# Performance work log

Hardware: AMD Instinct MI355X
Metric: run time of the kernel (lower is better)

## Reference

```python
import jax, jax.numpy as jnp
import numpy as np

COMMITMENT_COST = 0.25


def setup_inputs() -> dict:
    key = jax.random.key(0)
    k1, k2 = jax.random.split(key)
    inputs = jax.random.normal(k1, (64, 1024, 128), dtype=jnp.float32)
    # torch.rand init -> uniform [0, 1)
    codewords = jax.random.uniform(k2, (1024, 128), dtype=jnp.float32)
    return {"inputs": inputs, "codewords": codewords}


def reference(inputs, codewords):
    sg = jax.lax.stop_gradient
    D = codewords.shape[-1]
    flat = inputs.reshape(-1, D)  # (N, D)
    distances = (
        jnp.sum(flat * flat, axis=1, keepdims=True)
        - 2.0 * flat @ codewords.T
        + jnp.sum(codewords * codewords, axis=1)
    )  # (N, K)
    encoding_indices = jnp.argmin(distances, axis=1)  # (N,)
    quantized = codewords[encoding_indices].reshape(inputs.shape)

    quantizing_loss = jnp.mean((sg(quantized) - inputs) ** 2)
    commitment_loss = jnp.mean((quantized - sg(inputs)) ** 2)
    loss = quantizing_loss + COMMITMENT_COST * commitment_loss

    # straight-through estimator
    quantized = inputs + sg(quantized - inputs)
    return quantized, encoding_indices[:, None], loss
```

## Files before the change

kernel.cpp:

```cpp
#include <hip/hip_runtime.h>
#include <stdint.h>


typedef short     bf16x8 __attribute__((ext_vector_type(8)));
typedef float     f32x4  __attribute__((ext_vector_type(4)));
typedef unsigned short u16x8 __attribute__((ext_vector_type(8)));
typedef unsigned short u16x2 __attribute__((ext_vector_type(2)));

constexpr int N_ROWS = 65536;
constexpr int K_CODES = 1024;
constexpr int D = 128;
constexpr float MARGIN = 0.03f;

__device__ __forceinline__ unsigned short f32_to_bf16_rn(float f) {
    unsigned u = __float_as_uint(f);
    unsigned r = (u + 0x7FFFu + ((u >> 16) & 1u)) >> 16;
    return (unsigned short)r;
}
__device__ __forceinline__ float bf16_to_f32(unsigned short h) {
    return __uint_as_float(((unsigned)h) << 16);
}

__device__ __forceinline__ void gload_lds16(const void* g, void* l) {
    __builtin_amdgcn_global_load_lds(
        (const __attribute__((address_space(1))) unsigned int*)g,
        (__attribute__((address_space(3))) unsigned int*)l, 16, 0, 0);
}

__global__ __launch_bounds__(64) void vq_prep_cw(const float* __restrict__ cw,
                                                 unsigned short* __restrict__ Cp,
                                                 float* __restrict__ cnorm,
                                                 int* __restrict__ rcnt) {
    const int k = blockIdx.x;
    const int lane = threadIdx.x;
    float2 v = reinterpret_cast<const float2*>(cw + (size_t)k * D)[lane];
    float s = v.x * v.x + v.y * v.y;
#pragma unroll
    for (int off = 32; off; off >>= 1) s += __shfl_down(s, off, 64);
    if (lane == 0) cnorm[k] = s;
    if (lane == 0 && k == 0) *rcnt = 0;

    unsigned short hx = f32_to_bf16_rn(v.x), hy = f32_to_bf16_rn(v.y);
    unsigned short lx = f32_to_bf16_rn(v.x - bf16_to_f32(hx));
    unsigned short ly = f32_to_bf16_rn(v.y - bf16_to_f32(hy));
    size_t off0 = (size_t)k * D + lane * 2;
    u16x2 hv; hv[0] = hx; hv[1] = hy;
    u16x2 lv; lv[0] = lx; lv[1] = ly;
    *reinterpret_cast<u16x2*>(Cp + off0) = hv;
    *reinterpret_cast<u16x2*>(Cp + 131072 + off0) = lv;
}

__global__ __launch_bounds__(256, 3) void vq_argmin_mfma(
    const float* __restrict__ x,
    const unsigned short* __restrict__ Cp,
    const float* __restrict__ cnorm,
    float* __restrict__ half_bv,
    float* __restrict__ half_bv2,
    int* __restrict__ half_bi,
    float* __restrict__ xnorm) {
    __shared__ unsigned char Bs[2][2][8192];

    const int tid = threadIdx.x;
    const int wave = tid >> 6;
    const int lane = tid & 63;
    const int l15 = lane & 15;
    const int lg = lane >> 4;
    const int tile = blockIdx.x >> 1;
    const int khalf = blockIdx.x & 1;
    const int wrow = tile * 128 + wave * 32;

    const char* Cpb = reinterpret_cast<const char*>(Cp);
    auto stageB = [&](int c, int b) {
#pragma unroll
        for (int u = 0; u < 4; ++u) {
            int t = wave * 4 + u;
            int pl = t >> 3;
            int cwl = (t & 7) * 4 + lg;
            int q = l15 * 16;
            const char* src = Cpb + pl * 262144 + khalf * 131072
                              + ((size_t)(c * 32 + cwl)) * 256 + (q ^ ((cwl & 7) << 4));
            void* dst = (void*)&Bs[b][pl][(t & 7) * 1024];
            gload_lds16(src, dst);
        }
    };
    stageB(0, 0);

    bf16x8 A[2][4][2];
    float xn[2] = {0.f, 0.f};
#pragma unroll
    for (int r2 = 0; r2 < 2; ++r2) {
        const float* xr0 = x + (size_t)(wrow + r2 * 16 + l15) * D;
#pragma unroll
        for (int s = 0; s < 4; ++s) {
            const float4* xf = reinterpret_cast<const float4*>(xr0 + s * 32 + lg * 8);
            float4 f0 = xf[0];
            float4 f1 = xf[1];
            float in[8] = {f0.x, f0.y, f0.z, f0.w, f1.x, f1.y, f1.z, f1.w};
            u16x8 hv, lv;
#pragma unroll
            for (int e = 0; e < 8; ++e) {
                xn[r2] += in[e] * in[e];
                unsigned short h = f32_to_bf16_rn(in[e]);
                hv[e] = h;
                lv[e] = f32_to_bf16_rn(in[e] - bf16_to_f32(h));
            }
            A[r2][s][0] = *reinterpret_cast<bf16x8*>(&hv);
            A[r2][s][1] = *reinterpret_cast<bf16x8*>(&lv);
        }
    }
#pragma unroll
    for (int r2 = 0; r2 < 2; ++r2) {
        xn[r2] += __shfl_xor(xn[r2], 16, 64);
        xn[r2] += __shfl_xor(xn[r2], 32, 64);
        if (khalf == 0 && lg == 0) xnorm[wrow + r2 * 16 + l15] = xn[r2];
    }

    float bv[2][4], bv2[2][4];
    int bi_[2][4];
#pragma unroll
    for (int r2 = 0; r2 < 2; ++r2)
#pragma unroll
        for (int i = 0; i < 4; ++i) { bv[r2][i] = 3.4e38f; bv2[r2][i] = 3.4e38f; bi_[r2][i] = 0; }

    const int cb = l15 * 256;
    const int swz = (l15 & 7) << 4;
    int kb[4];
#pragma unroll
    for (int s = 0; s < 4; ++s) kb[s] = (s * 64 + lg * 16) ^ swz;

    asm volatile("s_waitcnt vmcnt(0)" ::: "memory");
    __syncthreads();

    for (int c = 0; c < 16; ++c) {
        const int buf = c & 1;
        if (c < 15) stageB(c + 1, buf ^ 1);

        f32x4 acc[2][2];
#pragma unroll
        for (int r2 = 0; r2 < 2; ++r2)
#pragma unroll
            for (int j = 0; j < 2; ++j) acc[r2][j] = (f32x4)(0.f);

#pragma unroll
        for (int s = 0; s < 4; ++s) {
            bf16x8 bh[2], bl[2];
#pragma unroll
            for (int j = 0; j < 2; ++j) {
                int ad = j * 4096 + cb + kb[s];
                bh[j] = *reinterpret_cast<const bf16x8*>(&Bs[buf][0][ad]);
                bl[j] = *reinterpret_cast<const bf16x8*>(&Bs[buf][1][ad]);
            }
#pragma unroll
            for (int r2 = 0; r2 < 2; ++r2)
#pragma unroll
                for (int j = 0; j < 2; ++j) {
                    acc[r2][j] = __builtin_amdgcn_mfma_f32_16x16x32_bf16(
                        A[r2][s][0], bh[j], acc[r2][j], 0, 0, 0);
                    acc[r2][j] = __builtin_amdgcn_mfma_f32_16x16x32_bf16(
                        A[r2][s][0], bl[j], acc[r2][j], 0, 0, 0);
                    acc[r2][j] = __builtin_amdgcn_mfma_f32_16x16x32_bf16(
                        A[r2][s][1], bh[j], acc[r2][j], 0, 0, 0);
                }
        }

#pragma unroll
        for (int j = 0; j < 2; ++j) {
            int col = khalf * 512 + c * 32 + j * 16 + l15;
            float cn = cnorm[col];
#pragma unroll
            for (int r2 = 0; r2 < 2; ++r2)
#pragma unroll
                for (int i = 0; i < 4; ++i) {
                    float sc = cn - 2.f * acc[r2][j][i];
                    if (sc < bv[r2][i]) {
                        bv2[r2][i] = bv[r2][i];
                        bv[r2][i] = sc;
                        bi_[r2][i] = col;
                    } else if (sc < bv2[r2][i]) {
                        bv2[r2][i] = sc;
                    }
                }
        }
        asm volatile("s_waitcnt vmcnt(0)" ::: "memory");
        __syncthreads();
    }

#pragma unroll
    for (int r2 = 0; r2 < 2; ++r2)
#pragma unroll
        for (int i = 0; i < 4; ++i) {
            float v = bv[r2][i], v2 = bv2[r2][i];
            int ix = bi_[r2][i];
#pragma unroll
            for (int off = 1; off < 16; off <<= 1) {
                float ov = __shfl_xor(v, off, 64);
                float ov2 = __shfl_xor(v2, off, 64);
                int oi = __shfl_xor(ix, off, 64);
                float nv2 = fminf(fminf(v2, ov2), fmaxf(v, ov));
                if (ov < v || (ov == v && oi < ix)) { v = ov; ix = oi; }
                v2 = nv2;
            }
            if (l15 == 0) {
                int row = wrow + r2 * 16 + lg * 4 + i;
                int o = khalf * N_ROWS + row;
                half_bv[o] = v;
                half_bv2[o] = v2;
                half_bi[o] = ix;
            }
        }
}

__global__ __launch_bounds__(256) void vq_merge(const float* __restrict__ cw,
                                                const float* __restrict__ half_bv,
                                                const float* __restrict__ half_bv2,
                                                const int* __restrict__ half_bi,
                                                const float* __restrict__ xnorm,
                                                float* __restrict__ out_idx_f,
                                                float* __restrict__ qout,
                                                float* __restrict__ rowloss,
                                                int* __restrict__ rcnt,
                                                int* __restrict__ rrows) {
    const int t = threadIdx.x;
    const int row = blockIdx.x * 8 + (t >> 5);
    const int d4 = t & 31;

    float v0 = half_bv[row], v0b = half_bv2[row];
    int i0 = half_bi[row];
    float v1 = half_bv[N_ROWS + row], v1b = half_bv2[N_ROWS + row];
    int i1 = half_bi[N_ROWS + row];

    bool take0 = (v0 < v1) || (v0 == v1 && i0 <= i1);
    float best = take0 ? v0 : v1;
    int bidx = take0 ? i0 : i1;
    float second = take0 ? fminf(v1, v0b) : fminf(v0, v1b);

    float4 q4 = reinterpret_cast<const float4*>(cw)[(size_t)bidx * 32 + d4];
    reinterpret_cast<float4*>(qout)[(size_t)row * 32 + d4] = q4;

    if (d4 == 0) {
        out_idx_f[row] = (float)bidx;
        rowloss[row] = xnorm[row] + best;
        if (second - best < MARGIN) {
            int p = atomicAdd(rcnt, 1);
            rrows[p] = row;
        }
    }
}

__global__ __launch_bounds__(256) void vq_repair(const float* __restrict__ x,
                                                 const float* __restrict__ cw,
                                                 const float* __restrict__ cnorm,
                                                 const float* __restrict__ xnorm,
                                                 const int* __restrict__ rcnt,
                                                 const int* __restrict__ rrows,
                                                 float* __restrict__ out_idx_f,
                                                 float* __restrict__ qout,
                                                 float* __restrict__ rowloss) {
    __shared__ float xs[16][132];
    __shared__ int rowids[16];
    __shared__ float sval[16][16];
    __shared__ int sidx[16][16];
    __shared__ int fidx[16];

    const int t = threadIdx.x;
    const int count = *rcnt;
    const float4* cw4 = reinterpret_cast<const float4*>(cw);

    for (int g = blockIdx.x; g * 16 < count; g += 256) {
        int nrows = min(16, count - g * 16);
        __syncthreads();
        if (t < 16) rowids[t] = rrows[g * 16 + (t < nrows ? t : 0)];
        __syncthreads();
        for (int i = t; i < 512; i += 256) {
            int r = i >> 5, d4 = i & 31;
            *reinterpret_cast<float4*>(&xs[r][d4 * 4]) =
                reinterpret_cast<const float4*>(x)[(size_t)rowids[r] * 32 + d4];
        }
        __syncthreads();

        const int r = t & 15;
        const int qq = t >> 4;
        float bv = 3.4e38f;
        int bi = 0;
#pragma unroll 2
        for (int kt = 0; kt < 8; ++kt) {
            float a[8] = {0.f, 0.f, 0.f, 0.f, 0.f, 0.f, 0.f, 0.f};
            int k0 = qq * 64 + kt * 8;
            for (int d4 = 0; d4 < 32; ++d4) {
                float4 xv = *reinterpret_cast<const float4*>(&xs[r][d4 * 4]);
#pragma unroll
                for (int kk = 0; kk < 8; ++kk) {
                    float4 cv = cw4[(size_t)(k0 + kk) * 32 + d4];
                    a[kk] += xv.x * cv.x + xv.y * cv.y + xv.z * cv.z + xv.w * cv.w;
                }
            }
#pragma unroll
            for (int kk = 0; kk < 8; ++kk) {
                int k = k0 + kk;
                float sc = cnorm[k] - 2.f * a[kk];
                if (sc < bv) { bv = sc; bi = k; }
            }
        }
        sval[r][qq] = bv;
        sidx[r][qq] = bi;
        __syncthreads();
        if (t < 16) {
            float fv = sval[t][0];
            int fi = sidx[t][0];
#pragma unroll
            for (int q2 = 1; q2 < 16; ++q2) {
                float v = sval[t][q2];
                int ii = sidx[t][q2];
                if (v < fv || (v == fv && ii < fi)) { fv = v; fi = ii; }
            }
            fidx[t] = fi;
            if (t < nrows) {
                int row = rowids[t];
                out_idx_f[row] = (float)fi;
                rowloss[row] = xnorm[row] + fv;
            }
        }
        __syncthreads();
        for (int i = t; i < 512; i += 256) {
            int rr = i >> 5, d4 = i & 31;
            float4 q4 = cw4[(size_t)fidx[rr] * 32 + d4];
            reinterpret_cast<float4*>(qout)[(size_t)rowids[rr] * 32 + d4] = q4;
        }
    }
}

__global__ __launch_bounds__(1024) void vq_loss_final(const float* __restrict__ rowloss,
                                                      float* __restrict__ out_loss) {
    double s = 0.0;
    for (int i = threadIdx.x; i < N_ROWS; i += 1024) s += (double)rowloss[i];
#pragma unroll
    for (int off = 32; off; off >>= 1) s += __shfl_down(s, off, 64);
    __shared__ double wsum[16];
    if ((threadIdx.x & 63) == 0) wsum[threadIdx.x >> 6] = s;
    __syncthreads();
    if (threadIdx.x == 0) {
        double tot = 0.0;
#pragma unroll
        for (int i = 0; i < 16; ++i) tot += wsum[i];
        *out_loss = (float)(tot * (1.25 / (double)((size_t)N_ROWS * D)));
    }
}

extern "C" void kernel_launch(void* const* d_in, const int* in_sizes, int n_in,
                              void* d_out, int out_size, void* d_ws, size_t ws_size,
                              hipStream_t stream) {
    const float* x = (const float*)d_in[0];
    const float* cw = (const float*)d_in[1];

    float* qout = (float*)d_out;
    float* out_idx_f = qout + (size_t)N_ROWS * D;
    float* out_loss = out_idx_f + N_ROWS;

    char* w = (char*)d_ws;
    unsigned short* Cp = (unsigned short*)w;          w += 524288;
    float* cnorm = (float*)w;                         w += 4096;
    int* rcnt = (int*)w;                              w += 256;
    int* rrows = (int*)w;                             w += 262144;
    float* half_bv = (float*)w;                       w += 524288;
    float* half_bv2 = (float*)w;                      w += 524288;
    int* half_bi = (int*)w;                           w += 524288;
    float* xnorm = (float*)w;                         w += 262144;
    float* rowloss = (float*)w;                       w += 262144;

    vq_prep_cw<<<K_CODES, 64, 0, stream>>>(cw, Cp, cnorm, rcnt);
    vq_argmin_mfma<<<(N_ROWS / 128) * 2, 256, 0, stream>>>(
        x, Cp, cnorm, half_bv, half_bv2, half_bi, xnorm);
    vq_merge<<<N_ROWS / 8, 256, 0, stream>>>(
        cw, half_bv, half_bv2, half_bi, xnorm, out_idx_f, qout, rowloss, rcnt, rrows);
    vq_repair<<<256, 256, 0, stream>>>(
        x, cw, cnorm, xnorm, rcnt, rrows, out_idx_f, qout, rowloss);
    vq_loss_final<<<1, 1024, 0, stream>>>(rowloss, out_loss);
}
```

Before: 256.5 us.

## Triple-buffer codebook staging, fuse loss reduction into merge/repair, shrink repair margin

The argmin kernel moves from double to triple buffering of codebook chunks. It waits with a partial vmcnt and raises wave priority around the MFMA block, so loads run further ahead of compute. The merge kernel handles 256 rows per block and accumulates the loss sum with a double atomic. Repair blocks add their delta to the same accumulator, and the final loss kernel becomes a single scalar write. The repair margin drops from 0.03 to 0.01, so fewer rows are rechecked in fp32, with some risk of index mismatches for near-ties given the bf16x3 precision.

```diff
diff --git a/kernel.cpp b/kernel.cpp
--- a/kernel.cpp
+++ b/kernel.cpp
@@ -10,7 +10,7 @@
 constexpr int N_ROWS = 65536;
 constexpr int K_CODES = 1024;
 constexpr int D = 128;
-constexpr float MARGIN = 0.03f;
+constexpr float MARGIN = 0.01f;
 
 __device__ __forceinline__ unsigned short f32_to_bf16_rn(float f) {
     unsigned u = __float_as_uint(f);
@@ -30,7 +30,8 @@
 __global__ __launch_bounds__(64) void vq_prep_cw(const float* __restrict__ cw,
                                                  unsigned short* __restrict__ Cp,
                                                  float* __restrict__ cnorm,
-                                                 int* __restrict__ rcnt) {
+                                                 int* __restrict__ rcnt,
+                                                 double* __restrict__ acc) {
     const int k = blockIdx.x;
     const int lane = threadIdx.x;
     float2 v = reinterpret_cast<const float2*>(cw + (size_t)k * D)[lane];
@@ -38,7 +39,7 @@
 #pragma unroll
     for (int off = 32; off; off >>= 1) s += __shfl_down(s, off, 64);
     if (lane == 0) cnorm[k] = s;
-    if (lane == 0 && k == 0) *rcnt = 0;
+    if (lane == 0 && k == 0) { *rcnt = 0; *acc = 0.0; }
 
     unsigned short hx = f32_to_bf16_rn(v.x), hy = f32_to_bf16_rn(v.y);
     unsigned short lx = f32_to_bf16_rn(v.x - bf16_to_f32(hx));
@@ -58,7 +59,7 @@
     float* __restrict__ half_bv2,
     int* __restrict__ half_bi,
     float* __restrict__ xnorm) {
-    __shared__ unsigned char Bs[2][2][8192];
+    __shared__ unsigned char Bs[3][2][8192];
 
     const int tid = threadIdx.x;
     const int wave = tid >> 6;
@@ -115,6 +116,8 @@
         if (khalf == 0 && lg == 0) xnorm[wrow + r2 * 16 + l15] = xn[r2];
     }
 
+    stageB(1, 1);
+
     float bv[2][4], bv2[2][4];
     int bi_[2][4];
 #pragma unroll
@@ -128,19 +131,14 @@
 #pragma unroll
     for (int s = 0; s < 4; ++s) kb[s] = (s * 64 + lg * 16) ^ swz;
 
-    asm volatile("s_waitcnt vmcnt(0)" ::: "memory");
-    __syncthreads();
-
-    for (int c = 0; c < 16; ++c) {
-        const int buf = c & 1;
-        if (c < 15) stageB(c + 1, buf ^ 1);
-
+    auto computeChunk = [&](int c, int buf) {
         f32x4 acc[2][2];
 #pragma unroll
         for (int r2 = 0; r2 < 2; ++r2)
 #pragma unroll
             for (int j = 0; j < 2; ++j) acc[r2][j] = (f32x4)(0.f);
 
+        __builtin_amdgcn_s_setprio(1);
 #pragma unroll
         for (int s = 0; s < 4; ++s) {
             bf16x8 bh[2], bl[2];
@@ -162,6 +160,7 @@
                         A[r2][s][1], bh[j], acc[r2][j], 0, 0, 0);
                 }
         }
+        __builtin_amdgcn_s_setprio(0);
 
 #pragma unroll
         for (int j = 0; j < 2; ++j) {
@@ -181,9 +180,21 @@
                     }
                 }
         }
-        asm volatile("s_waitcnt vmcnt(0)" ::: "memory");
-        __syncthreads();
-    }
+    };
+
+    int cur = 0;
+    for (int c = 0; c < 15; ++c) {
+        asm volatile("s_waitcnt vmcnt(4)\n\ts_barrier" ::: "memory");
+        if (c < 14) {
+            int stg = cur + 2;
+            if (stg >= 3) stg -= 3;
+            stageB(c + 2, stg);
+        }
+        computeChunk(c, cur);
+        cur = (cur == 2) ? 0 : cur + 1;
+    }
+    asm volatile("s_waitcnt vmcnt(0)\n\ts_barrier" ::: "memory");
+    computeChunk(15, cur);
 
 #pragma unroll
     for (int r2 = 0; r2 < 2; ++r2)
@@ -219,32 +230,44 @@
                                                 float* __restrict__ qout,
                                                 float* __restrict__ rowloss,
                                                 int* __restrict__ rcnt,
-                                                int* __restrict__ rrows) {
+                                                int* __restrict__ rrows,
+                                                double* __restrict__ acc) {
     const int t = threadIdx.x;
-    const int row = blockIdx.x * 8 + (t >> 5);
     const int d4 = t & 31;
-
-    float v0 = half_bv[row], v0b = half_bv2[row];
-    int i0 = half_bi[row];
-    float v1 = half_bv[N_ROWS + row], v1b = half_bv2[N_ROWS + row];
-    int i1 = half_bi[N_ROWS + row];
-
-    bool take0 = (v0 < v1) || (v0 == v1 && i0 <= i1);
-    float best = take0 ? v0 : v1;
-    int bidx = take0 ? i0 : i1;
-    float second = take0 ? fminf(v1, v0b) : fminf(v0, v1b);
-
-    float4 q4 = reinterpret_cast<const float4*>(cw)[(size_t)bidx * 32 + d4];
-    reinterpret_cast<float4*>(qout)[(size_t)row * 32 + d4] = q4;
-
-    if (d4 == 0) {
-        out_idx_f[row] = (float)bidx;
-        rowloss[row] = xnorm[row] + best;
-        if (second - best < MARGIN) {
-            int p = atomicAdd(rcnt, 1);
-            rrows[p] = row;
-        }
-    }
+    double lsum = 0.0;
+
+    for (int it = 0; it < 32; ++it) {
+        int row = blockIdx.x * 256 + it * 8 + (t >> 5);
+        float v0 = half_bv[row], v0b = half_bv2[row];
+        int i0 = half_bi[row];
+        float v1 = half_bv[N_ROWS + row], v1b = half_bv2[N_ROWS + row];
+        int i1 = half_bi[N_ROWS + row];
+
+        bool take0 = (v0 < v1) || (v0 == v1 && i0 <= i1);
+        float best = take0 ? v0 : v1;
+        int bidx = take0 ? i0 : i1;
+        float second = take0 ? fminf(v1, v0b) : fminf(v0, v1b);
+
+        float4 q4 = reinterpret_cast<const float4*>(cw)[(size_t)bidx * 32 + d4];
+        reinterpret_cast<float4*>(qout)[(size_t)row * 32 + d4] = q4;
+
+        if (d4 == 0) {
+            out_idx_f[row] = (float)bidx;
+            float rl = xnorm[row] + best;
+            rowloss[row] = rl;
+            lsum += (double)rl;
+            if (second - best < MARGIN) {
+                int p = atomicAdd(rcnt, 1);
+                rrows[p] = row;
+            }
+        }
+    }
+#pragma unroll
+    for (int off = 32; off; off >>= 1) lsum += __shfl_down(lsum, off, 64);
+    __shared__ double wsum[4];
+    if ((t & 63) == 0) wsum[t >> 6] = lsum;
+    __syncthreads();
+    if (t == 0) atomicAdd(acc, wsum[0] + wsum[1] + wsum[2] + wsum[3]);
 }
 
 __global__ __launch_bounds__(256) void vq_repair(const float* __restrict__ x,
@@ -255,7 +278,8 @@
                                                  const int* __restrict__ rrows,
                                                  float* __restrict__ out_idx_f,
                                                  float* __restrict__ qout,
-                                                 float* __restrict__ rowloss) {
+                                                 float* __restrict__ rowloss,
+                                                 double* __restrict__ acc) {
     __shared__ float xs[16][132];
     __shared__ int rowids[16];
     __shared__ float sval[16][16];
@@ -265,8 +289,9 @@
     const int t = threadIdx.x;
     const int count = *rcnt;
     const float4* cw4 = reinterpret_cast<const float4*>(cw);
-
-    for (int g = blockIdx.x; g * 16 < count; g += 256) {
+    double dsum = 0.0;
+
+    for (int g = blockIdx.x; g * 16 < count; g += 512) {
         int nrows = min(16, count - g * 16);
         __syncthreads();
         if (t < 16) rowids[t] = rrows[g * 16 + (t < nrows ? t : 0)];
@@ -317,7 +342,10 @@
             if (t < nrows) {
                 int row = rowids[t];
                 out_idx_f[row] = (float)fi;
-                rowloss[row] = xnorm[row] + fv;
+                float nrl = xnorm[row] + fv;
+                float orl = rowloss[row];
+                rowloss[row] = nrl;
+                dsum += (double)nrl - (double)orl;
             }
         }
         __syncthreads();
@@ -327,23 +355,20 @@
             reinterpret_cast<float4*>(qout)[(size_t)rowids[rr] * 32 + d4] = q4;
         }
     }
-}
-
-__global__ __launch_bounds__(1024) void vq_loss_final(const float* __restrict__ rowloss,
-                                                      float* __restrict__ out_loss) {
-    double s = 0.0;
-    for (int i = threadIdx.x; i < N_ROWS; i += 1024) s += (double)rowloss[i];
-#pragma unroll
-    for (int off = 32; off; off >>= 1) s += __shfl_down(s, off, 64);
-    __shared__ double wsum[16];
-    if ((threadIdx.x & 63) == 0) wsum[threadIdx.x >> 6] = s;
+#pragma unroll
+    for (int off = 32; off; off >>= 1) dsum += __shfl_down(dsum, off, 64);
+    __shared__ double wsum[4];
+    if ((t & 63) == 0) wsum[t >> 6] = dsum;
     __syncthreads();
-    if (threadIdx.x == 0) {
-        double tot = 0.0;
-#pragma unroll
-        for (int i = 0; i < 16; ++i) tot += wsum[i];
-        *out_loss = (float)(tot * (1.25 / (double)((size_t)N_ROWS * D)));
-    }
+    if (t == 0) {
+        double b = wsum[0] + wsum[1] + wsum[2] + wsum[3];
+        if (b != 0.0) atomicAdd(acc, b);
+    }
+}
+
+__global__ void vq_loss_final(const double* __restrict__ acc,
+                              float* __restrict__ out_loss) {
+    *out_loss = (float)(*acc * (1.25 / (double)((size_t)N_ROWS * D)));
 }
 
 extern "C" void kernel_launch(void* const* d_in, const int* in_sizes, int n_in,
@@ -359,7 +384,8 @@
     char* w = (char*)d_ws;
     unsigned short* Cp = (unsigned short*)w;          w += 524288;
     float* cnorm = (float*)w;                         w += 4096;
-    int* rcnt = (int*)w;                              w += 256;
+    int* rcnt = (int*)w;                              w += 16;
+    double* acc = (double*)w;                         w += 240;
     int* rrows = (int*)w;                             w += 262144;
     float* half_bv = (float*)w;                       w += 524288;
     float* half_bv2 = (float*)w;                      w += 524288;
@@ -367,12 +393,12 @@
     float* xnorm = (float*)w;                         w += 262144;
     float* rowloss = (float*)w;                       w += 262144;
 
-    vq_prep_cw<<<K_CODES, 64, 0, stream>>>(cw, Cp, cnorm, rcnt);
+    vq_prep_cw<<<K_CODES, 64, 0, stream>>>(cw, Cp, cnorm, rcnt, acc);
     vq_argmin_mfma<<<(N_ROWS / 128) * 2, 256, 0, stream>>>(
         x, Cp, cnorm, half_bv, half_bv2, half_bi, xnorm);
-    vq_merge<<<N_ROWS / 8, 256, 0, stream>>>(
-        cw, half_bv, half_bv2, half_bi, xnorm, out_idx_f, qout, rowloss, rcnt, rrows);
-    vq_repair<<<256, 256, 0, stream>>>(
-        x, cw, cnorm, xnorm, rcnt, rrows, out_idx_f, qout, rowloss);
-    vq_loss_final<<<1, 1024, 0, stream>>>(rowloss, out_loss);
-}
+    vq_merge<<<N_ROWS / 256, 256, 0, stream>>>(
+        cw, half_bv, half_bv2, half_bi, xnorm, out_idx_f, qout, rowloss, rcnt, rrows, acc);
+    vq_repair<<<512, 256, 0, stream>>>(
+        x, cw, cnorm, xnorm, rcnt, rrows, out_idx_f, qout, rowloss, acc);
+    vq_loss_final<<<1, 1, 0, stream>>>(acc, out_loss);
+}
```

After: 255.2 us. No clear change (-0.5%).
